# Kernel optimization log

Hardware: AMD Instinct MI355X
Metric: run time of the kernel (lower is better)

Reference implementation:

```python
import jax, jax.numpy as jnp
import numpy as np

ALPHA = 1.702
LIMIT = 7.0


def setup_inputs() -> dict:
    key = jax.random.key(0)
    ks = jax.random.split(key, 7)
    B, S, H, D, E, TOPK = 2, 2048, 2048, 2048, 8, 4
    T = B * S
    hidden_states = jax.random.normal(ks[0], (B, S, H), dtype=jnp.float32)
    gate_up_proj = jax.random.normal(ks[1], (E, H, 2 * D), dtype=jnp.float32) * 0.02
    gate_up_proj_bias = jax.random.normal(ks[2], (E, 2 * D), dtype=jnp.float32) * 0.02
    down_proj = jax.random.normal(ks[3], (E, D, H), dtype=jnp.float32) * 0.02
    down_proj_bias = jax.random.normal(ks[4], (E, H), dtype=jnp.float32) * 0.02
    rw = jax.random.uniform(ks[5], (T, E), dtype=jnp.float32)
    routing_weights = rw / jnp.sum(rw, axis=-1, keepdims=True)
    router_indices = jax.random.randint(ks[6], (T, TOPK), 0, E, dtype=jnp.int64)
    return {
        "hidden_states": hidden_states,
        "gate_up_proj": gate_up_proj,
        "gate_up_proj_bias": gate_up_proj_bias,
        "down_proj": down_proj,
        "down_proj_bias": down_proj_bias,
        "routing_weights": routing_weights,
        "router_indices": router_indices,
    }


def geglu(gate_up):
    # interleaved layout: gate = [..., 0::2], up = [..., 1::2]
    gate = gate_up[..., 0::2]
    up = gate_up[..., 1::2]
    gate = jnp.minimum(gate, LIMIT)
    up = jnp.clip(up, -LIMIT, LIMIT)
    glu = gate * jax.nn.sigmoid(gate * ALPHA)
    return (up + 1.0) * glu


def reference(hidden_states, gate_up_proj, gate_up_proj_bias, down_proj,
              down_proj_bias, routing_weights, router_indices):
    B, S, H = hidden_states.shape
    x = hidden_states.reshape(-1, H)  # [T, H]
    # per-expert batched GEMM: [E, T, 2D]
    gate_up = jnp.einsum('th,ehd->etd', x, gate_up_proj) + gate_up_proj_bias[:, None, :]
    act = geglu(gate_up)  # [E, T, D]
    out = jnp.einsum('etd,edh->eth', act, down_proj) + down_proj_bias[:, None, :]
    # weight by router probs and sum over experts
    out = out * routing_weights.T[:, :, None]  # [E, T, H]
    out = jnp.sum(out, axis=0)
    return out.reshape(B, S, H)
```

## Files before the change

kernel.cpp:

```cpp
#include <hip/hip_runtime.h>
#include <hip/hip_bf16.h>

#define ALPHA 1.702f
#define GLIMIT 7.0f

typedef __attribute__((ext_vector_type(4))) float f32x4;
typedef __attribute__((ext_vector_type(4))) short short4v;
typedef __attribute__((ext_vector_type(8))) __bf16 bf16x8;
typedef __attribute__((ext_vector_type(8))) short short8;

typedef __attribute__((address_space(3))) unsigned int as3_uint;
typedef const __attribute__((address_space(1))) unsigned int as1_uint;

__device__ __forceinline__ void async_copy16(void* lds, const void* g) {
    __builtin_amdgcn_global_load_lds((as1_uint*)g, (as3_uint*)lds, 16, 0, 0);
}

__device__ __forceinline__ short f2bf(float f) {
    unsigned u = __float_as_uint(f);
    unsigned r = (u + 0x7fffu + ((u >> 16) & 1u)) >> 16;
    return (short)r;
}

__global__ void cvt_bf16_kernel(const float* __restrict__ src,
                                short* __restrict__ dst, int n4) {
    int i = blockIdx.x * blockDim.x + threadIdx.x;
    if (i < n4) {
        float4 v = reinterpret_cast<const float4*>(src)[i];
        short4 o;
        o.x = f2bf(v.x); o.y = f2bf(v.y); o.z = f2bf(v.z); o.w = f2bf(v.w);
        reinterpret_cast<short4*>(dst)[i] = o;
    }
}

__global__ void transpose_cvt(const float* __restrict__ src,
                              short* __restrict__ dst, int R, int C, int perm) {
    __shared__ float t[64][65];
    const int z  = blockIdx.z;
    const int c0 = blockIdx.x * 64;
    const int r0 = blockIdx.y * 64;
    const float* s = src + (size_t)z * R * C;
    short* d = dst + (size_t)z * R * C;
    const int tid = threadIdx.x;
#pragma unroll
    for (int i = 0; i < 16; ++i) {
        int idx = i * 256 + tid;
        int r = idx >> 6, c = idx & 63;
        t[r][c] = s[(size_t)(r0 + r) * C + c0 + c];
    }
    __syncthreads();
#pragma unroll
    for (int i = 0; i < 16; ++i) {
        int idx = i * 256 + tid;
        int r = idx >> 6, c = idx & 63;
        int rr = c0 + r;
        int rloc = rr & 255;
        int rp = perm ? ((rr & ~255) | ((rloc & 1) << 7) | (rloc >> 1)) : rr;
        d[(size_t)rp * R + r0 + c] = f2bf(t[c][r]);
    }
}


struct Gemm1TSrc {
    const short* A; const short* B;
    __device__ __forceinline__ const short* operator()(int t, int h) const {
        int e = (t >> 5) & 7;
        size_t ko = (size_t)(t & 31) << 6;
        if (h & 2) return B + ((size_t)(h & 1) << 18) + ko;
        return A + ((size_t)e << 23) + ((size_t)(h & 1) << 18) + ko;
    }
};

struct Gemm2Src {
    const short* act; const short* wdt; size_t aoff, boff; int kh;
    __device__ __forceinline__ const short* operator()(int t, int h) const {
        int g = (kh << 7) + t;
        int e = g >> 5;
        size_t ko = (size_t)(g & 31) << 6;
        if (h & 2) return wdt + ((size_t)e << 22) + boff + ((size_t)(h & 1) << 18) + ko;
        return act + ((size_t)e << 23) + aoff + ((size_t)(h & 1) << 18) + ko;
    }
};

#define PH_BAR()  __builtin_amdgcn_s_barrier()
#define PH_LGKM() do { asm volatile("s_waitcnt lgkmcnt(0)" ::: "memory"); \
                       __builtin_amdgcn_sched_barrier(0); } while (0)
#define VMW(n)    asm volatile("s_waitcnt vmcnt(" #n ")" ::: "memory")

template <int NT, int SEG, bool DRAIN, typename Src, typename Epi>
__device__ __forceinline__ void gemm_8phase(const Src& src, char* smem,
                                            f32x4 (&acc)[8][4], const Epi& epi) {
    const int tid  = threadIdx.x;
    const int lane = tid & 63;
    const int wid  = tid >> 6;
    const int wr   = wid >> 2;
    const int wcol = wid & 3;
    const int lhi  = lane >> 4;
    const int llo  = lane & 15;

    auto stage = [&](int buf, int h, const short* g) {
        char* dst = smem + buf * 65536 + h * 16384;
        {
            int c = tid, r = c >> 3, s = (c & 7) ^ (r & 7);
            async_copy16(dst + c * 16, g + (size_t)r * 2048 + s * 8);
        }
        {
            int c = tid + 512, r = c >> 3, s = (c & 7) ^ (r & 7);
            async_copy16(dst + c * 16, g + (size_t)r * 2048 + s * 8);
        }
    };
    auto ldfrag = [&](int buf, int h, int row, int slot) {
        return *(const bf16x8*)(smem + buf * 65536 + h * 16384 + row * 128 +
                                ((slot ^ (row & 7)) << 4));
    };

    stage(0, 0, src(0, 0)); stage(0, 2, src(0, 2));
    stage(0, 3, src(0, 3)); stage(0, 1, src(0, 1));
    stage(1, 0, src(1, 0)); stage(1, 2, src(1, 2)); stage(1, 3, src(1, 3));
    VMW(8);
    PH_BAR();

    bf16x8 a[4][2], b[4][2];
#pragma unroll
    for (int n = 0; n < 2; ++n) {
        int row = wcol * 32 + n * 16 + llo;
        b[n][0] = ldfrag(0, 2, row, lhi);
        b[n][1] = ldfrag(0, 2, row, 4 + lhi);
    }

    for (int t = 0; t < NT; ++t) {
        const int cur = t & 1, nxt = cur ^ 1;
#pragma unroll
        for (int m = 0; m < 4; ++m) {
            int row = wr * 64 + m * 16 + llo;
            a[m][0] = ldfrag(cur, 0, row, lhi);
            a[m][1] = ldfrag(cur, 0, row, 4 + lhi);
        }
        if (t + 1 < NT) stage(nxt, 1, src(t + 1, 1));
        PH_BAR(); PH_LGKM();
        __builtin_amdgcn_s_setprio(1);
#pragma unroll
        for (int m = 0; m < 4; ++m)
#pragma unroll
            for (int n = 0; n < 2; ++n)
#pragma unroll
                for (int ks = 0; ks < 2; ++ks)
                    acc[m][n] = __builtin_amdgcn_mfma_f32_16x16x32_bf16(
                        a[m][ks], b[n][ks], acc[m][n], 0, 0, 0);
        __builtin_amdgcn_s_setprio(0);
        PH_BAR();
#pragma unroll
        for (int n = 0; n < 2; ++n) {
            int row = wcol * 32 + n * 16 + llo;
            b[2 + n][0] = ldfrag(cur, 3, row, lhi);
            b[2 + n][1] = ldfrag(cur, 3, row, 4 + lhi);
        }
        if (t + 2 < NT) { stage(cur, 0, src(t + 2, 0)); VMW(10); }
        else if (t + 1 < NT) { VMW(8); }
        else { VMW(0); }
        PH_BAR(); PH_LGKM();
        __builtin_amdgcn_s_setprio(1);
#pragma unroll
        for (int m = 0; m < 4; ++m)
#pragma unroll
            for (int n = 2; n < 4; ++n)
#pragma unroll
                for (int ks = 0; ks < 2; ++ks)
                    acc[m][n] = __builtin_amdgcn_mfma_f32_16x16x32_bf16(
                        a[m][ks], b[n][ks], acc[m][n], 0, 0, 0);
        __builtin_amdgcn_s_setprio(0);
        PH_BAR();
#pragma unroll
        for (int m = 0; m < 4; ++m) {
            int row = wr * 64 + m * 16 + llo;
            a[m][0] = ldfrag(cur, 1, row, lhi);
            a[m][1] = ldfrag(cur, 1, row, 4 + lhi);
        }
        if (t + 2 < NT) stage(cur, 2, src(t + 2, 2));
        PH_BAR(); PH_LGKM();
        __builtin_amdgcn_s_setprio(1);
#pragma unroll
        for (int m = 0; m < 4; ++m)
#pragma unroll
            for (int n = 0; n < 2; ++n)
#pragma unroll
                for (int ks = 0; ks < 2; ++ks)
                    acc[4 + m][n] = __builtin_amdgcn_mfma_f32_16x16x32_bf16(
                        a[m][ks], b[n][ks], acc[4 + m][n], 0, 0, 0);
        __builtin_amdgcn_s_setprio(0);
        PH_BAR();
        if (t + 2 < NT) { stage(cur, 3, src(t + 2, 3)); VMW(8); }
        else if (t + 1 < NT) { VMW(2); }
        else { VMW(0); }
        PH_BAR(); PH_LGKM();
        __builtin_amdgcn_s_setprio(1);
        if (t + 1 < NT) {
#pragma unroll
            for (int n = 0; n < 2; ++n) {
                int row = wcol * 32 + n * 16 + llo;
                b[n][0] = ldfrag(nxt, 2, row, lhi);
                b[n][1] = ldfrag(nxt, 2, row, 4 + lhi);
            }
        }
#pragma unroll
        for (int m = 0; m < 4; ++m)
#pragma unroll
            for (int n = 2; n < 4; ++n)
#pragma unroll
                for (int ks = 0; ks < 2; ++ks)
                    acc[4 + m][n] = __builtin_amdgcn_mfma_f32_16x16x32_bf16(
                        a[m][ks], b[n][ks], acc[4 + m][n], 0, 0, 0);
        __builtin_amdgcn_s_setprio(0);
        PH_BAR();
        if (((t + 1) & (SEG - 1)) == 0) {
            epi(t / SEG, acc);
            if (t + 1 < NT) {
                if (DRAIN) { VMW(0); }
#pragma unroll
                for (int m = 0; m < 8; ++m)
#pragma unroll
                    for (int n = 0; n < 4; ++n)
                        acc[m][n] = (f32x4){0.f, 0.f, 0.f, 0.f};
            }
        }
    }
}

__global__ __launch_bounds__(512, 2) void gemm1_main(
    const short* __restrict__ xb, const short* __restrict__ wgutp,
    const float* __restrict__ bias, const float* __restrict__ rwp,
    short* __restrict__ act) {
    __shared__ __align__(16) char smem[131072];
    __shared__ float rws2[2048];
    __shared__ float bias2[2048];
    const int bid = blockIdx.x;
    const int xcd = bid & 7, j = bid >> 3;
    const int t0 = (((xcd & 3) << 2) + (j & 3)) << 8;
    const int p0 = (((xcd >> 2) << 3) + (j >> 2)) << 8;
    const int tid  = threadIdx.x;
    const int lane = tid & 63;
    const int wid  = tid >> 6;
    const int wr = wid >> 2, wcol = wid & 3;
    const int lhi = lane >> 4, llo = lane & 15;

    ((float4*)rws2)[tid] = ((const float4*)(rwp + (size_t)t0 * 8))[tid];
    {
        int idx = tid << 2;
        int ei = idx >> 8, c = idx & 255;
        ((float4*)bias2)[tid] =
            *(const float4*)(bias + (size_t)ei * 4096 + p0 + c);
    }

    f32x4 acc[8][4];
#pragma unroll
    for (int m = 0; m < 8; ++m)
#pragma unroll
        for (int n = 0; n < 4; ++n) acc[m][n] = (f32x4){0.f, 0.f, 0.f, 0.f};

    Gemm1TSrc src{ wgutp + (size_t)p0 * 2048, xb + (size_t)t0 * 2048 };
    const int dbase = (p0 >> 1) + wr * 64;

    auto epi = [&](int s, f32x4 (&ac)[8][4]) {
        int e = s & 7;
        short* acte = act + ((size_t)e << 23);
#pragma unroll
        for (int m = 0; m < 4; ++m) {
            float bg[4], bu[4];
#pragma unroll
            for (int q = 0; q < 4; ++q) {
                int jj = wr * 64 + m * 16 + (lhi << 2) + q;
                bg[q] = bias2[(e << 8) + 2 * jj];
                bu[q] = bias2[(e << 8) + 2 * jj + 1];
            }
            int dc0 = dbase + m * 16 + (lhi << 2);
#pragma unroll
            for (int n = 0; n < 4; ++n) {
                int tloc = ((n >> 1) << 7) + wcol * 32 + ((n & 1) << 4) + llo;
                float w = rws2[tloc * 8 + e];
                short4v o;
#pragma unroll
                for (int q = 0; q < 4; ++q) {
                    float g = ac[m][n][q] + bg[q];
                    float u = ac[4 + m][n][q] + bu[q];
                    g = fminf(g, GLIMIT);
                    u = fmaxf(fminf(u, GLIMIT), -GLIMIT);
                    float glu = g / (1.f + __expf(-ALPHA * g));
                    o[q] = f2bf((u + 1.f) * glu * w);
                }
                __builtin_nontemporal_store(
                    o, (short4v*)(acte + (size_t)(t0 + tloc) * 2048 + dc0));
            }
        }
    };
    gemm_8phase<256, 32, true>(src, smem, acc, epi);
}

__global__ __launch_bounds__(512, 2) void gemm2_8ph(
    const short* __restrict__ act, const short* __restrict__ wdt,
    float* __restrict__ out, float* __restrict__ part) {
    __shared__ __align__(16) char smem[131072];
    const int kh = blockIdx.z;
    int flat = blockIdx.x + (blockIdx.y << 3);
    int swz = (flat & 7) * 16 + (flat >> 3);
    const int n0 = (swz & 7) * 256;
    const int m0 = (swz >> 3) * 256;
    const int tid  = threadIdx.x;
    const int lane = tid & 63;
    const int wid  = tid >> 6;
    const int wr = wid >> 2, wcol = wid & 3;

    f32x4 acc[8][4];
#pragma unroll
    for (int m = 0; m < 8; ++m)
#pragma unroll
        for (int n = 0; n < 4; ++n) acc[m][n] = (f32x4){0.f, 0.f, 0.f, 0.f};

    Gemm2Src src{ act, wdt, (size_t)m0 * 2048, (size_t)n0 * 2048, kh };
    float* dst = (kh == 0) ? out : part;

    auto epi = [&](int, f32x4 (&ac)[8][4]) {
#pragma unroll
        for (int m = 0; m < 8; ++m) {
            int row = m0 + (m >> 2) * 128 + wr * 64 + (m & 3) * 16 + ((lane >> 4) << 2);
#pragma unroll
            for (int n = 0; n < 4; ++n) {
                int col = n0 + (n >> 1) * 128 + wcol * 32 + (n & 1) * 16 + (lane & 15);
#pragma unroll
                for (int q = 0; q < 4; ++q)
                    dst[(size_t)(row + q) * 2048 + col] = ac[m][n][q];
            }
        }
    };
    gemm_8phase<128, 128, false>(src, smem, acc, epi);
}

__global__ __launch_bounds__(256) void reduce_bias(
    const float* __restrict__ p1, const float* __restrict__ rw,
    const float* __restrict__ bd, float* __restrict__ out) {
    const int t = blockIdx.x;
    const int tid = threadIdx.x;
    float rwv[8];
#pragma unroll
    for (int e = 0; e < 8; ++e) rwv[e] = rw[(size_t)t * 8 + e];
    size_t base = (size_t)t * 2048;
#pragma unroll
    for (int i = 0; i < 2; ++i) {
        int h = (tid + i * 256) * 4;
        f32x4 o = *(const f32x4*)(out + base + h);
        f32x4 p = *(const f32x4*)(p1 + base + h);
        o += p;
#pragma unroll
        for (int e = 0; e < 8; ++e) {
            f32x4 bb = *(const f32x4*)(bd + e * 2048 + h);
            o += rwv[e] * bb;
        }
        *(f32x4*)(out + base + h) = o;
    }
}

extern "C" void kernel_launch(void* const* d_in, const int* in_sizes, int n_in,
                              void* d_out, int out_size, void* d_ws, size_t ws_size,
                              hipStream_t stream) {
    const float* x   = (const float*)d_in[0];
    const float* wgu = (const float*)d_in[1];
    const float* bgu = (const float*)d_in[2];
    const float* wd  = (const float*)d_in[3];
    const float* bd  = (const float*)d_in[4];
    const float* rw  = (const float*)d_in[5];
    float* out = (float*)d_out;

    char* ws = (char*)d_ws;
    short* xb   = (short*)(ws);
    short* wgut = (short*)(ws + 16777216);
    float* p1   = (float*)(ws + 16777216);
    short* wdt  = (short*)(ws + 150994944);
    short* actb = (short*)(ws + 218103808);

    cvt_bf16_kernel<<<8192, 256, 0, stream>>>(x, xb, 2097152);
    transpose_cvt<<<dim3(64, 32, 8), 256, 0, stream>>>(wgu, wgut, 2048, 4096, 1);
    transpose_cvt<<<dim3(32, 32, 8), 256, 0, stream>>>(wd, wdt, 2048, 2048, 0);
    gemm1_main<<<256, 512, 0, stream>>>(xb, wgut, bgu, rw, actb);
    gemm2_8ph<<<dim3(8, 16, 2), 512, 0, stream>>>(actb, wdt, out, p1);
    reduce_bias<<<4096, 256, 0, stream>>>(p1, rw, bd, out);
}
```

Baseline: 915.0 us.

## Triple-buffer A1 LDS slot to prefetch it two iterations ahead

Reorganizes the GEMM LDS staging into named slots and gives the second A half a three-way rotating buffer. Its global-to-LDS copy for tile t+2 can then be issued at the start of an iteration instead of just in time for t+1. One intermediate vmcnt wait is removed to loosen the schedule. To make room within the same LDS footprint, the routing-weight and bias tables are no longer staged in shared memory; the epilogue reads them directly from global memory. That trades the LDS space for extra global loads in the epilogue and makes the wait-count bookkeeping more fragile.

```diff
diff --git a/kernel.cpp b/kernel.cpp
--- a/kernel.cpp
+++ b/kernel.cpp
@@ -61,6 +61,11 @@
 }
 
 
+#define SLOT_A0(p) ((p) * 16384)
+#define SLOT_B0(p) (32768 + (p) * 16384)
+#define SLOT_B1(p) (65536 + (p) * 16384)
+#define SLOT_A1(r) (98304 + (r) * 16384)
+
 struct Gemm1TSrc {
     const short* A; const short* B;
     __device__ __forceinline__ const short* operator()(int t, int h) const {
@@ -75,7 +80,7 @@
     const short* act; const short* wdt; size_t aoff, boff; int kh;
     __device__ __forceinline__ const short* operator()(int t, int h) const {
         int g = (kh << 7) + t;
-        int e = g >> 5;
+        int e = (g >> 5) & 7;
         size_t ko = (size_t)(g & 31) << 6;
         if (h & 2) return wdt + ((size_t)e << 22) + boff + ((size_t)(h & 1) << 18) + ko;
         return act + ((size_t)e << 23) + aoff + ((size_t)(h & 1) << 18) + ko;
@@ -98,8 +103,8 @@
     const int lhi  = lane >> 4;
     const int llo  = lane & 15;
 
-    auto stage = [&](int buf, int h, const short* g) {
-        char* dst = smem + buf * 65536 + h * 16384;
+    auto stage = [&](int off, const short* g) {
+        char* dst = smem + off;
         {
             int c = tid, r = c >> 3, s = (c & 7) ^ (r & 7);
             async_copy16(dst + c * 16, g + (size_t)r * 2048 + s * 8);
@@ -109,14 +114,15 @@
             async_copy16(dst + c * 16, g + (size_t)r * 2048 + s * 8);
         }
     };
-    auto ldfrag = [&](int buf, int h, int row, int slot) {
-        return *(const bf16x8*)(smem + buf * 65536 + h * 16384 + row * 128 +
+    auto ldfrag = [&](int off, int row, int slot) {
+        return *(const bf16x8*)(smem + off + row * 128 +
                                 ((slot ^ (row & 7)) << 4));
     };
 
-    stage(0, 0, src(0, 0)); stage(0, 2, src(0, 2));
-    stage(0, 3, src(0, 3)); stage(0, 1, src(0, 1));
-    stage(1, 0, src(1, 0)); stage(1, 2, src(1, 2)); stage(1, 3, src(1, 3));
+    stage(SLOT_A0(0), src(0, 0)); stage(SLOT_B0(0), src(0, 2));
+    stage(SLOT_B1(0), src(0, 3)); stage(SLOT_A1(0), src(0, 1));
+    stage(SLOT_A0(1), src(1, 0)); stage(SLOT_B0(1), src(1, 2));
+    stage(SLOT_B1(1), src(1, 3)); stage(SLOT_A1(1), src(1, 1));
     VMW(8);
     PH_BAR();
 
@@ -124,19 +130,21 @@
 #pragma unroll
     for (int n = 0; n < 2; ++n) {
         int row = wcol * 32 + n * 16 + llo;
-        b[n][0] = ldfrag(0, 2, row, lhi);
-        b[n][1] = ldfrag(0, 2, row, 4 + lhi);
-    }
-
+        b[n][0] = ldfrag(SLOT_B0(0), row, lhi);
+        b[n][1] = ldfrag(SLOT_B0(0), row, 4 + lhi);
+    }
+
+    int a1s = 0;
     for (int t = 0; t < NT; ++t) {
         const int cur = t & 1, nxt = cur ^ 1;
+        const int a1t = (a1s >= 1) ? a1s - 1 : a1s + 2;
 #pragma unroll
         for (int m = 0; m < 4; ++m) {
             int row = wr * 64 + m * 16 + llo;
-            a[m][0] = ldfrag(cur, 0, row, lhi);
-            a[m][1] = ldfrag(cur, 0, row, 4 + lhi);
-        }
-        if (t + 1 < NT) stage(nxt, 1, src(t + 1, 1));
+            a[m][0] = ldfrag(SLOT_A0(cur), row, lhi);
+            a[m][1] = ldfrag(SLOT_A0(cur), row, 4 + lhi);
+        }
+        if (t + 2 < NT) stage(SLOT_A1(a1t), src(t + 2, 1));
         PH_BAR(); PH_LGKM();
         __builtin_amdgcn_s_setprio(1);
 #pragma unroll
@@ -152,12 +160,10 @@
 #pragma unroll
         for (int n = 0; n < 2; ++n) {
             int row = wcol * 32 + n * 16 + llo;
-            b[2 + n][0] = ldfrag(cur, 3, row, lhi);
-            b[2 + n][1] = ldfrag(cur, 3, row, 4 + lhi);
-        }
-        if (t + 2 < NT) { stage(cur, 0, src(t + 2, 0)); VMW(10); }
-        else if (t + 1 < NT) { VMW(8); }
-        else { VMW(0); }
+            b[2 + n][0] = ldfrag(SLOT_B1(cur), row, lhi);
+            b[2 + n][1] = ldfrag(SLOT_B1(cur), row, 4 + lhi);
+        }
+        if (t + 2 < NT) stage(SLOT_A0(cur), src(t + 2, 0));
         PH_BAR(); PH_LGKM();
         __builtin_amdgcn_s_setprio(1);
 #pragma unroll
@@ -173,10 +179,10 @@
 #pragma unroll
         for (int m = 0; m < 4; ++m) {
             int row = wr * 64 + m * 16 + llo;
-            a[m][0] = ldfrag(cur, 1, row, lhi);
-            a[m][1] = ldfrag(cur, 1, row, 4 + lhi);
-        }
-        if (t + 2 < NT) stage(cur, 2, src(t + 2, 2));
+            a[m][0] = ldfrag(SLOT_A1(a1s), row, lhi);
+            a[m][1] = ldfrag(SLOT_A1(a1s), row, 4 + lhi);
+        }
+        if (t + 2 < NT) stage(SLOT_B0(cur), src(t + 2, 2));
         PH_BAR(); PH_LGKM();
         __builtin_amdgcn_s_setprio(1);
 #pragma unroll
@@ -189,8 +195,7 @@
                         a[m][ks], b[n][ks], acc[4 + m][n], 0, 0, 0);
         __builtin_amdgcn_s_setprio(0);
         PH_BAR();
-        if (t + 2 < NT) { stage(cur, 3, src(t + 2, 3)); VMW(8); }
-        else if (t + 1 < NT) { VMW(2); }
+        if (t + 2 < NT) { stage(SLOT_B1(cur), src(t + 2, 3)); VMW(8); }
         else { VMW(0); }
         PH_BAR(); PH_LGKM();
         __builtin_amdgcn_s_setprio(1);
@@ -198,8 +203,8 @@
 #pragma unroll
             for (int n = 0; n < 2; ++n) {
                 int row = wcol * 32 + n * 16 + llo;
-                b[n][0] = ldfrag(nxt, 2, row, lhi);
-                b[n][1] = ldfrag(nxt, 2, row, 4 + lhi);
+                b[n][0] = ldfrag(SLOT_B0(nxt), row, lhi);
+                b[n][1] = ldfrag(SLOT_B0(nxt), row, 4 + lhi);
             }
         }
 #pragma unroll
@@ -223,6 +228,7 @@
                         acc[m][n] = (f32x4){0.f, 0.f, 0.f, 0.f};
             }
         }
+        a1s = (a1s == 2) ? 0 : a1s + 1;
     }
 }
 
@@ -230,9 +236,7 @@
     const short* __restrict__ xb, const short* __restrict__ wgutp,
     const float* __restrict__ bias, const float* __restrict__ rwp,
     short* __restrict__ act) {
-    __shared__ __align__(16) char smem[131072];
-    __shared__ float rws2[2048];
-    __shared__ float bias2[2048];
+    __shared__ __align__(16) char smem[147456];
     const int bid = blockIdx.x;
     const int xcd = bid & 7, j = bid >> 3;
     const int t0 = (((xcd & 3) << 2) + (j & 3)) << 8;
@@ -243,14 +247,6 @@
     const int wr = wid >> 2, wcol = wid & 3;
     const int lhi = lane >> 4, llo = lane & 15;
 
-    ((float4*)rws2)[tid] = ((const float4*)(rwp + (size_t)t0 * 8))[tid];
-    {
-        int idx = tid << 2;
-        int ei = idx >> 8, c = idx & 255;
-        ((float4*)bias2)[tid] =
-            *(const float4*)(bias + (size_t)ei * 4096 + p0 + c);
-    }
-
     f32x4 acc[8][4];
 #pragma unroll
     for (int m = 0; m < 8; ++m)
@@ -263,20 +259,21 @@
     auto epi = [&](int s, f32x4 (&ac)[8][4]) {
         int e = s & 7;
         short* acte = act + ((size_t)e << 23);
+        const float* be = bias + ((size_t)e << 12) + p0;
 #pragma unroll
         for (int m = 0; m < 4; ++m) {
             float bg[4], bu[4];
 #pragma unroll
             for (int q = 0; q < 4; ++q) {
                 int jj = wr * 64 + m * 16 + (lhi << 2) + q;
-                bg[q] = bias2[(e << 8) + 2 * jj];
-                bu[q] = bias2[(e << 8) + 2 * jj + 1];
+                bg[q] = be[2 * jj];
+                bu[q] = be[2 * jj + 1];
             }
             int dc0 = dbase + m * 16 + (lhi << 2);
 #pragma unroll
             for (int n = 0; n < 4; ++n) {
                 int tloc = ((n >> 1) << 7) + wcol * 32 + ((n & 1) << 4) + llo;
-                float w = rws2[tloc * 8 + e];
+                float w = rwp[(size_t)(t0 + tloc) * 8 + e];
                 short4v o;
 #pragma unroll
                 for (int q = 0; q < 4; ++q) {
@@ -298,7 +295,7 @@
 __global__ __launch_bounds__(512, 2) void gemm2_8ph(
     const short* __restrict__ act, const short* __restrict__ wdt,
     float* __restrict__ out, float* __restrict__ part) {
-    __shared__ __align__(16) char smem[131072];
+    __shared__ __align__(16) char smem[147456];
     const int kh = blockIdx.z;
     int flat = blockIdx.x + (blockIdx.y << 3);
     int swz = (flat & 7) * 16 + (flat >> 3);
```

Measured after the change: 908.7 us. No clear change (-0.7%).
